# Kernel optimization log

Measured on AMD Instinct MI355X. Metric: run time of the kernel, lower is better.

## Reference

```python
import jax, jax.numpy as jnp
import numpy as np

BETA = 0.9        # LIF membrane decay
THRESHOLD = 1.0   # LIF firing threshold
SURROGATE_K = 25.0  # superspike surrogate slope (spyx default)

@jax.custom_vjp
def spike(u):
    return (u > 0.0).astype(u.dtype)

def _spike_fwd(u):
    return spike(u), u

def _spike_bwd(u, g):
    # superspike surrogate gradient
    return (g / (1.0 + SURROGATE_K * jnp.abs(u)) ** 2,)

spike.defvjp(_spike_fwd, _spike_bwd)

def lif(V, I):
    # leaky integrate, fire, reset-by-subtraction (spyx snn.LIF semantics)
    V = BETA * V + I
    s = spike(V - THRESHOLD)
    V = V - s * THRESHOLD
    return s, V

def setup_inputs() -> dict:
    key = jax.random.key(0)
    ks = jax.random.split(key, 9)
    T, B, D, H, L = 512, 64, 1024, 2048, 256
    def lin(k, fan_in, shape):
        return jax.random.normal(k, shape, jnp.float32) / np.sqrt(fan_in)
    return {
        "x_seq": jax.random.normal(ks[0], (T, B, D), jnp.float32),
        "W_enc": lin(ks[1], D, (D, H)), "b_enc": jnp.zeros((H,), jnp.float32),
        "W_lat": lin(ks[2], H, (H, L)), "b_lat": jnp.zeros((L,), jnp.float32),
        "W_dec": lin(ks[3], L, (L, H)), "b_dec": jnp.zeros((H,), jnp.float32),
        "W_rec": lin(ks[4], H, (H, D)), "b_rec": jnp.zeros((D,), jnp.float32),
    }

def reference(x_seq, W_enc, b_enc, W_lat, b_lat, W_dec, b_dec, W_rec, b_rec):
    T, B, D = x_seq.shape
    H, L = W_enc.shape[1], W_lat.shape[1]
    V0 = (jnp.zeros((B, H), x_seq.dtype),
          jnp.zeros((B, L), x_seq.dtype),
          jnp.zeros((B, H), x_seq.dtype))

    def step(carry, x_t):
        Ve, Vl, Vd = carry
        s_enc, Ve = lif(Ve, x_t @ W_enc + b_enc)      # [B,H]
        z_t, Vl = lif(Vl, s_enc @ W_lat + b_lat)      # [B,L]
        s_dec, Vd = lif(Vd, z_t @ W_dec + b_dec)      # [B,H]
        recon_t = s_dec @ W_rec + b_rec               # [B,D]
        sr_t = jnp.stack([jnp.mean(s_enc), jnp.mean(z_t), jnp.mean(s_dec)])
        return (Ve, Vl, Vd), (recon_t, z_t, sr_t)

    _, (recon_seq, latent_seq, sr_seq) = jax.lax.scan(step, V0, x_seq)
    recon = jnp.mean(recon_seq, axis=0)  # readout='mean'
    spike_rate = jnp.mean(sr_seq, axis=0)
    recon_err = jnp.mean(jnp.abs(recon_seq - x_seq))
    return recon, recon_seq, latent_seq, spike_rate, recon_err
```

## Files before the change

### kernel.cpp

```cpp
#include <hip/hip_runtime.h>


#define T_STEPS 512
#define BB 64
#define DD 1024
#define HH 2048
#define LL 256

template<typename AT>
__global__ __launch_bounds__(256) void gemm_panel(
    const AT* __restrict__ A, const float* __restrict__ Bm,
    const float* __restrict__ bias, float* __restrict__ C,
    int M, int N, int K)
{
  __shared__ float As[2][8][128];
  __shared__ float Bs[2][8][128];
  const int tid = threadIdx.x;
  const int tx = tid & 15, ty = tid >> 4;
  const int row0 = blockIdx.y * 128, col0 = blockIdx.x * 128;
  const int lar = tid >> 1;
  const int lak = (tid & 1) * 4;
  const int lbk = tid >> 5;
  const int lbn = (tid & 31) * 4;

  float acc[8][8] = {};
  float pacc[8][8] = {};
  const int KT = K >> 3;

  float a4[4];
  float4 b4;
  auto fetch = [&](int kt) {
    if constexpr (sizeof(AT) == 1) {
      uchar4 u = *(const uchar4*)(A + (size_t)(row0 + lar) * K + kt * 8 + lak);
      a4[0] = u.x; a4[1] = u.y; a4[2] = u.z; a4[3] = u.w;
    } else {
      float4 f = *(const float4*)((const float*)A + (size_t)(row0 + lar) * K + kt * 8 + lak);
      a4[0] = f.x; a4[1] = f.y; a4[2] = f.z; a4[3] = f.w;
    }
    b4 = *(const float4*)(Bm + (size_t)(kt * 8 + lbk) * N + col0 + lbn);
  };

  fetch(0);
  As[0][lak + 0][lar] = a4[0]; As[0][lak + 1][lar] = a4[1];
  As[0][lak + 2][lar] = a4[2]; As[0][lak + 3][lar] = a4[3];
  *(float4*)&Bs[0][lbk][lbn] = b4;
  __syncthreads();

  for (int kt = 0; kt < KT; ++kt) {
    const int cur = kt & 1;
    if (kt > 0 && (kt & 63) == 0) {
      #pragma unroll
      for (int i = 0; i < 8; ++i)
        #pragma unroll
        for (int j = 0; j < 8; ++j) {
          acc[i][j] = __fadd_rn(acc[i][j], pacc[i][j]);
          pacc[i][j] = 0.0f;
        }
    }
    if (kt + 1 < KT) {
      fetch(kt + 1);
      const int nxt = cur ^ 1;
      As[nxt][lak + 0][lar] = a4[0]; As[nxt][lak + 1][lar] = a4[1];
      As[nxt][lak + 2][lar] = a4[2]; As[nxt][lak + 3][lar] = a4[3];
      *(float4*)&Bs[nxt][lbk][lbn] = b4;
    }
    #pragma unroll
    for (int k = 0; k < 8; ++k) {
      float av[8], bv[8];
      *(float4*)&av[0] = *(const float4*)&As[cur][k][ty * 8];
      *(float4*)&av[4] = *(const float4*)&As[cur][k][ty * 8 + 4];
      *(float4*)&bv[0] = *(const float4*)&Bs[cur][k][tx * 8];
      *(float4*)&bv[4] = *(const float4*)&Bs[cur][k][tx * 8 + 4];
      #pragma unroll
      for (int i = 0; i < 8; ++i)
        #pragma unroll
        for (int j = 0; j < 8; ++j)
          pacc[i][j] = fmaf(av[i], bv[j], pacc[i][j]);
    }
    __syncthreads();
  }

  #pragma unroll
  for (int i = 0; i < 8; ++i) {
    float bb[8];
    *(float4*)&bb[0] = *(const float4*)&bias[col0 + tx * 8];
    *(float4*)&bb[4] = *(const float4*)&bias[col0 + tx * 8 + 4];
    float o[8];
    #pragma unroll
    for (int j = 0; j < 8; ++j) {
      float tot = __fadd_rn(acc[i][j], pacc[i][j]);
      o[j] = __fadd_rn(tot, bb[j]);
    }
    const size_t r = (size_t)(row0 + ty * 8 + i) * N + col0 + tx * 8;
    *(float4*)&C[r] = *(const float4*)&o[0];
    *(float4*)&C[r + 4] = *(const float4*)&o[4];
  }
}

__global__ __launch_bounds__(256) void lif_scan(
    const float* __restrict__ I, float* __restrict__ V,
    unsigned char* __restrict__ S, float* __restrict__ latent,
    unsigned long long* __restrict__ cnt, int Tc, int NTOT)
{
  const int idx = blockIdx.x * 256 + threadIdx.x;
  float v = V[idx];
  unsigned c = 0;
  for (int t = 0; t < Tc; ++t) {
    v = fmaf(0.9f, v, I[(size_t)t * NTOT + idx]);
    const bool s = __fsub_rn(v, 1.0f) > 0.0f;
    if (s) v = __fsub_rn(v, 1.0f);
    S[(size_t)t * NTOT + idx] = (unsigned char)s;
    if (latent) latent[(size_t)t * NTOT + idx] = s ? 1.0f : 0.0f;
    c += (unsigned)s;
  }
  V[idx] = v;
  unsigned long long cc = c;
  for (int o = 32; o; o >>= 1) cc += __shfl_down(cc, o);
  if ((threadIdx.x & 63) == 0 && cc) atomicAdd(cnt, cc);
}

__global__ __launch_bounds__(256) void recon_mean_kernel(
    const float* __restrict__ rs, float* __restrict__ out)
{
  const int idx = blockIdx.x * 256 + threadIdx.x;
  double s = 0.0;
  for (int t = 0; t < T_STEPS; ++t) s += (double)rs[(size_t)t * 65536 + idx];
  out[idx] = (float)(s * (1.0 / 512.0));
}

__global__ __launch_bounds__(256) void err_kernel(
    const float* __restrict__ rs, const float* __restrict__ x,
    double* __restrict__ acc)
{
  const size_t N = (size_t)T_STEPS * BB * DD;
  double s = 0.0;
  for (size_t i = (size_t)blockIdx.x * 256 + threadIdx.x; i < N;
       i += (size_t)gridDim.x * 256)
    s += (double)fabsf(rs[i] - x[i]);
  for (int o = 32; o; o >>= 1) s += __shfl_down(s, o);
  __shared__ double wsum[4];
  if ((threadIdx.x & 63) == 0) wsum[threadIdx.x >> 6] = s;
  __syncthreads();
  if (threadIdx.x == 0) atomicAdd(acc, wsum[0] + wsum[1] + wsum[2] + wsum[3]);
}

__global__ void finalize_kernel(const double* __restrict__ acc,
                                const unsigned long long* __restrict__ cnt,
                                float* __restrict__ sr, float* __restrict__ err)
{
  if (threadIdx.x == 0) {
    sr[0] = (float)((double)cnt[0] / (512.0 * 64.0 * 2048.0));
    sr[1] = (float)((double)cnt[1] / (512.0 * 64.0 * 256.0));
    sr[2] = (float)((double)cnt[2] / (512.0 * 64.0 * 2048.0));
    err[0] = (float)(acc[0] / (512.0 * 64.0 * 1024.0));
  }
}

extern "C" void kernel_launch(void* const* d_in, const int* in_sizes, int n_in,
                              void* d_out, int out_size, void* d_ws, size_t ws_size,
                              hipStream_t stream) {
  const float* x    = (const float*)d_in[0];
  const float* Wenc = (const float*)d_in[1];
  const float* benc = (const float*)d_in[2];
  const float* Wlat = (const float*)d_in[3];
  const float* blat = (const float*)d_in[4];
  const float* Wdec = (const float*)d_in[5];
  const float* bdec = (const float*)d_in[6];
  const float* Wrec = (const float*)d_in[7];
  const float* brec = (const float*)d_in[8];

  float* out = (float*)d_out;
  float* recon     = out;
  float* recon_seq = out + 65536;
  float* latent    = recon_seq + (size_t)T_STEPS * BB * DD;
  float* sr        = latent + (size_t)T_STEPS * BB * LL;
  float* errp      = sr + 3;

  char* ws = (char*)d_ws;
  float* Ve = (float*)ws;
  float* Vl = (float*)(ws + 524288);
  float* Vd = (float*)(ws + 589824);
  unsigned long long* cnt = (unsigned long long*)(ws + 1114112);
  double* errAcc = (double*)(ws + 1114136);
  const size_t STATE = 1114368;

  unsigned char* Senc = (unsigned char*)(ws + STATE);
  unsigned char* Sdec = Senc;
  const size_t Z_OFF    = STATE + 67108864;
  unsigned char* Z      = (unsigned char*)(ws + Z_OFF);
  const size_t ILAT_OFF = Z_OFF + 8388608;
  float* Ilat           = (float*)(ws + ILAT_OFF);
  const size_t ICH_OFF  = ILAT_OFF + 33554432;
  float* Ichunk         = (float*)(ws + ICH_OFF);

  int Tc = 512;
  while (Tc > 2 && ICH_OFF + (size_t)Tc * 524288 > ws_size) Tc >>= 1;

  hipMemsetAsync(ws, 0, STATE, stream);

  for (int c0 = 0; c0 < T_STEPS; c0 += Tc) {
    gemm_panel<float><<<dim3(HH / 128, Tc * BB / 128), 256, 0, stream>>>(
        x + (size_t)c0 * BB * DD, Wenc, benc, Ichunk, Tc * BB, HH, DD);
    lif_scan<<<512, 256, 0, stream>>>(
        Ichunk, Ve, Senc + (size_t)c0 * BB * HH, nullptr, &cnt[0], Tc, BB * HH);
  }
  gemm_panel<unsigned char><<<dim3(LL / 128, T_STEPS * BB / 128), 256, 0, stream>>>(
      Senc, Wlat, blat, Ilat, T_STEPS * BB, LL, HH);
  lif_scan<<<64, 256, 0, stream>>>(
      Ilat, Vl, Z, latent, &cnt[1], T_STEPS, BB * LL);
  for (int c0 = 0; c0 < T_STEPS; c0 += Tc) {
    gemm_panel<unsigned char><<<dim3(HH / 128, Tc * BB / 128), 256, 0, stream>>>(
        Z + (size_t)c0 * BB * LL, Wdec, bdec, Ichunk, Tc * BB, HH, LL);
    lif_scan<<<512, 256, 0, stream>>>(
        Ichunk, Vd, Sdec + (size_t)c0 * BB * HH, nullptr, &cnt[2], Tc, BB * HH);
    gemm_panel<unsigned char><<<dim3(DD / 128, Tc * BB / 128), 256, 0, stream>>>(
        Sdec + (size_t)c0 * BB * HH, Wrec, brec,
        recon_seq + (size_t)c0 * BB * DD, Tc * BB, DD, HH);
  }

  recon_mean_kernel<<<256, 256, 0, stream>>>(recon_seq, recon);
  err_kernel<<<2048, 256, 0, stream>>>(recon_seq, x, errAcc);
  finalize_kernel<<<1, 64, 0, stream>>>(errAcc, cnt, sr, errp);
}
```

Before: 4.788 ms.

## Deepen GEMM K-tile to 16, split thread fragments to avoid LDS bank conflicts

The GEMM panel kernel now stages a K-depth of 16 per iteration instead of 8, and uses a single LDS buffer with register prefetch of the next tile in place of LDS double buffering. Each thread's 8x8 fragment is split into two 4-wide halves 64 apart, which reduces LDS bank conflicts on the float4 reads and makes the output stores more coalesced. The intent is fewer barriers per unit of K and less LDS conflict overhead. The cost is an extra barrier per iteration and less overlap between global loads and compute. The partial-sum flush interval moves from every 64 tiles to every 32, so the flush still happens every 512 K-elements.

Measured after the change: 5.735 ms. 19.8% more time.

```diff
diff --git a/kernel.cpp b/kernel.cpp
--- a/kernel.cpp
+++ b/kernel.cpp
@@ -13,42 +13,43 @@
     const float* __restrict__ bias, float* __restrict__ C,
     int M, int N, int K)
 {
-  __shared__ float As[2][8][128];
-  __shared__ float Bs[2][8][128];
+  __shared__ float As[16][128];
+  __shared__ float Bs[16][128];
   const int tid = threadIdx.x;
   const int tx = tid & 15, ty = tid >> 4;
   const int row0 = blockIdx.y * 128, col0 = blockIdx.x * 128;
   const int lar = tid >> 1;
-  const int lak = (tid & 1) * 4;
-  const int lbk = tid >> 5;
-  const int lbn = (tid & 31) * 4;
+  const int lak = (tid & 1) * 8;
+  const int lbk = tid >> 4;
+  const int lbn = (tid & 15) * 8;
 
   float acc[8][8] = {};
   float pacc[8][8] = {};
-  const int KT = K >> 3;
-
-  float a4[4];
-  float4 b4;
+  const int KT = K >> 4;
+
+  float a8[8];
+  float4 b40, b41;
   auto fetch = [&](int kt) {
     if constexpr (sizeof(AT) == 1) {
-      uchar4 u = *(const uchar4*)(A + (size_t)(row0 + lar) * K + kt * 8 + lak);
-      a4[0] = u.x; a4[1] = u.y; a4[2] = u.z; a4[3] = u.w;
+      unsigned long long w =
+          *(const unsigned long long*)(A + (size_t)(row0 + lar) * K + kt * 16 + lak);
+      #pragma unroll
+      for (int j = 0; j < 8; ++j) a8[j] = (float)((w >> (8 * j)) & 0xFFull);
     } else {
-      float4 f = *(const float4*)((const float*)A + (size_t)(row0 + lar) * K + kt * 8 + lak);
-      a4[0] = f.x; a4[1] = f.y; a4[2] = f.z; a4[3] = f.w;
-    }
-    b4 = *(const float4*)(Bm + (size_t)(kt * 8 + lbk) * N + col0 + lbn);
+      const float* ap = (const float*)A + (size_t)(row0 + lar) * K + kt * 16 + lak;
+      float4 f0 = *(const float4*)ap;
+      float4 f1 = *(const float4*)(ap + 4);
+      a8[0] = f0.x; a8[1] = f0.y; a8[2] = f0.z; a8[3] = f0.w;
+      a8[4] = f1.x; a8[5] = f1.y; a8[6] = f1.z; a8[7] = f1.w;
+    }
+    const float* bp = Bm + (size_t)(kt * 16 + lbk) * N + col0 + lbn;
+    b40 = *(const float4*)bp;
+    b41 = *(const float4*)(bp + 4);
   };
 
   fetch(0);
-  As[0][lak + 0][lar] = a4[0]; As[0][lak + 1][lar] = a4[1];
-  As[0][lak + 2][lar] = a4[2]; As[0][lak + 3][lar] = a4[3];
-  *(float4*)&Bs[0][lbk][lbn] = b4;
-  __syncthreads();
-
   for (int kt = 0; kt < KT; ++kt) {
-    const int cur = kt & 1;
-    if (kt > 0 && (kt & 63) == 0) {
+    if (kt > 0 && (kt & 31) == 0) {
       #pragma unroll
       for (int i = 0; i < 8; ++i)
         #pragma unroll
@@ -57,20 +58,19 @@
           pacc[i][j] = 0.0f;
         }
     }
-    if (kt + 1 < KT) {
-      fetch(kt + 1);
-      const int nxt = cur ^ 1;
-      As[nxt][lak + 0][lar] = a4[0]; As[nxt][lak + 1][lar] = a4[1];
-      As[nxt][lak + 2][lar] = a4[2]; As[nxt][lak + 3][lar] = a4[3];
-      *(float4*)&Bs[nxt][lbk][lbn] = b4;
-    }
     #pragma unroll
-    for (int k = 0; k < 8; ++k) {
+    for (int j = 0; j < 8; ++j) As[lak + j][lar] = a8[j];
+    *(float4*)&Bs[lbk][lbn] = b40;
+    *(float4*)&Bs[lbk][lbn + 4] = b41;
+    __syncthreads();
+    if (kt + 1 < KT) fetch(kt + 1);
+    #pragma unroll
+    for (int k = 0; k < 16; ++k) {
       float av[8], bv[8];
-      *(float4*)&av[0] = *(const float4*)&As[cur][k][ty * 8];
-      *(float4*)&av[4] = *(const float4*)&As[cur][k][ty * 8 + 4];
-      *(float4*)&bv[0] = *(const float4*)&Bs[cur][k][tx * 8];
-      *(float4*)&bv[4] = *(const float4*)&Bs[cur][k][tx * 8 + 4];
+      *(float4*)&av[0] = *(const float4*)&As[k][ty * 4];
+      *(float4*)&av[4] = *(const float4*)&As[k][64 + ty * 4];
+      *(float4*)&bv[0] = *(const float4*)&Bs[k][tx * 4];
+      *(float4*)&bv[4] = *(const float4*)&Bs[k][64 + tx * 4];
       #pragma unroll
       for (int i = 0; i < 8; ++i)
         #pragma unroll
@@ -80,20 +80,21 @@
     __syncthreads();
   }
 
+  float bb[8];
+  *(float4*)&bb[0] = *(const float4*)&bias[col0 + tx * 4];
+  *(float4*)&bb[4] = *(const float4*)&bias[col0 + 64 + tx * 4];
   #pragma unroll
   for (int i = 0; i < 8; ++i) {
-    float bb[8];
-    *(float4*)&bb[0] = *(const float4*)&bias[col0 + tx * 8];
-    *(float4*)&bb[4] = *(const float4*)&bias[col0 + tx * 8 + 4];
+    const int r = (i < 4) ? (ty * 4 + i) : (64 + ty * 4 + i - 4);
     float o[8];
     #pragma unroll
     for (int j = 0; j < 8; ++j) {
       float tot = __fadd_rn(acc[i][j], pacc[i][j]);
       o[j] = __fadd_rn(tot, bb[j]);
     }
-    const size_t r = (size_t)(row0 + ty * 8 + i) * N + col0 + tx * 8;
-    *(float4*)&C[r] = *(const float4*)&o[0];
-    *(float4*)&C[r + 4] = *(const float4*)&o[4];
+    const size_t base = (size_t)(row0 + r) * N + col0;
+    *(float4*)&C[base + tx * 4] = *(const float4*)&o[0];
+    *(float4*)&C[base + 64 + tx * 4] = *(const float4*)&o[4];
   }
 }
 
```
